# Kernel tuning notes

Measured on AMD Instinct MI355X. Metric: run time of the kernel, lower is better.

Reference implementation:

```python
import jax, jax.numpy as jnp
import numpy as np

DIM = 256
HEADS = 8
DK = DIM // HEADS
MLP_HID = 4 * DIM
EPS = 1e-5


def _ln(t, s, b):
    m = jnp.mean(t, axis=-1, keepdims=True)
    v = jnp.mean((t - m) ** 2, axis=-1, keepdims=True)
    return (t - m) / jnp.sqrt(v + EPS) * s + b


def setup_inputs() -> dict:
    key = jax.random.key(0)
    ks = jax.random.split(key, 32)
    B, N, C = 8, 128, DIM
    d = {}
    d["x"] = jax.random.normal(ks[0], (B, N, C), jnp.float32)
    d["y"] = jax.random.normal(ks[1], (B, N, N, C), jnp.float32)
    def lin(k, fi, fo):
        k1, k2 = jax.random.split(k)
        return (jax.random.normal(k1, (fi, fo), jnp.float32) * 0.02,
                jax.random.normal(k2, (fo,), jnp.float32) * 0.02)
    for i, nm in enumerate(["q", "k", "v", "e", "oe", "on"]):
        w, b = lin(ks[2 + i], C, C)
        d[f"W{nm}"], d[f"b{nm}"] = w, b
    for i, nm in enumerate(["mlp1", "mlp2"]):
        w1, b1 = lin(ks[10 + 2 * i], C, MLP_HID)
        w2, b2 = lin(ks[11 + 2 * i], MLP_HID, C)
        d[f"{nm}_w1"], d[f"{nm}_b1"] = w1, b1
        d[f"{nm}_w2"], d[f"{nm}_b2"] = w2, b2
    for i, nm in enumerate(["ln1", "ln3", "ln4", "ln5", "ln6"]):
        d[f"{nm}_s"] = jnp.ones((C,), jnp.float32)
        d[f"{nm}_b"] = jnp.zeros((C,), jnp.float32)
    return d


def reference(x, y, Wq, bq, Wk, bk, Wv, bv, We, be, Woe, boe, Won, bon,
              mlp1_w1, mlp1_b1, mlp1_w2, mlp1_b2,
              mlp2_w1, mlp2_b1, mlp2_w2, mlp2_b2,
              ln1_s, ln1_b, ln3_s, ln3_b, ln4_s, ln4_b,
              ln5_s, ln5_b, ln6_s, ln6_b):
    B, N, C = x.shape
    H, DKl = HEADS, DK

    x1 = _ln(x, ln1_s, ln1_b)

    # attention (elementwise q*k modulated by edge embeddings)
    q = (x1 @ Wq + bq).reshape(B, N, H, DKl)
    k = (x1 @ Wk + bk).reshape(B, N, H, DKl)
    v = (x1 @ Wv + bv).reshape(B, N, H, DKl)
    e = (y @ We + be).reshape(B, N, N, H, DKl)

    attn = q[:, :, None] * k[:, None, :]          # (B,N,N,H,DK)
    attn = attn / jnp.sqrt(jnp.float32(DKl))
    attn = attn * (e + 1.0) * e

    edge_out = attn.reshape(B, N, N, C) @ Woe + boe  # out_e
    p = jax.nn.softmax(attn, axis=2)                 # softmax over second n
    agg = jnp.einsum("bijhd,bjhd->bihd", p, v).reshape(B, N, C)
    node_out = agg @ Won + bon                       # out_n

    x2 = _ln(x1 + node_out, ln3_s, ln3_b)
    y2 = _ln(edge_out + y, ln4_s, ln4_b)

    mlp_x = jax.nn.relu(x2 @ mlp1_w1 + mlp1_b1) @ mlp1_w2 + mlp1_b2
    mlp_y = jax.nn.relu(y2 @ mlp2_w1 + mlp2_b1) @ mlp2_w2 + mlp2_b2

    x_out = _ln(x2 + mlp_x, ln5_s, ln5_b)
    y_out = _ln(y2 + mlp_y, ln6_s, ln6_b)
    return (x_out, y_out)
```

## Files before the change

### kernel.cpp

```cpp
#include <hip/hip_runtime.h>

#define CDIM 256
#define NSEQ 128
#define HID 1024
#define EPS 1e-5f
#define SCALE 0.17677669529663687f
#define ASTR 264
#define MROWS 32

typedef __attribute__((ext_vector_type(8))) short short8;
typedef __attribute__((ext_vector_type(4))) float f32x4;

static __device__ __forceinline__ unsigned short f2bf(float x) {
    unsigned u = __float_as_uint(x);
    u += 0x7fff + ((u >> 16) & 1);
    return (unsigned short)(u >> 16);
}
static __device__ __forceinline__ float bf2f(unsigned short h) {
    return __uint_as_float(((unsigned)h) << 16);
}

__global__ __launch_bounds__(256) void prep_all(
    const float* __restrict__ We, const float* __restrict__ Woe,
    const float* __restrict__ W1, const float* __restrict__ W2,
    unsigned short* __restrict__ WeH, unsigned short* __restrict__ WeL,
    unsigned short* __restrict__ WoH, unsigned short* __restrict__ W1H,
    unsigned short* __restrict__ W2H) {
    int blk = blockIdx.x;
    const float* W; unsigned short* H; unsigned short* L = nullptr;
    int N, ksBits, base;
    if (blk < 256)       { W = We;  H = WeH; L = WeL; N = 256;  ksBits = 3; base = 0; }
    else if (blk < 512)  { W = Woe; H = WoH; N = 256;  ksBits = 3; base = 256; }
    else if (blk < 1536) { W = W1;  H = W1H; N = 1024; ksBits = 3; base = 512; }
    else                 { W = W2;  H = W2H; N = 256;  ksBits = 5; base = 1536; }
    int idx = (blk - base) * 256 + threadIdx.x;
    int j = idx & 7, lane = (idx >> 3) & 63, rest = idx >> 9;
    int ks = rest & ((1 << ksBits) - 1), nt = rest >> ksBits;
    int n  = nt * 16 + (lane & 15);
    int kk = ks * 32 + ((lane >> 4) << 3) + j;
    float x = W[kk * N + n];
    unsigned short h = f2bf(x);
    H[idx] = h;
    if (L) L[idx] = f2bf(x - bf2f(h));
}

__global__ __launch_bounds__(256) void lnqkv_kernel(
    const float* __restrict__ x,
    const float* __restrict__ ln1s, const float* __restrict__ ln1b,
    const float* __restrict__ Wq, const float* __restrict__ bq,
    const float* __restrict__ Wk, const float* __restrict__ bk,
    const float* __restrict__ Wv, const float* __restrict__ bv,
    float* __restrict__ x1,
    float* __restrict__ q, float* __restrict__ k, float* __restrict__ v) {
    __shared__ float sX[4][CDIM];
    __shared__ float sMu[4], sRs[4];
    const int bi0 = blockIdx.x * 4, t = threadIdx.x;
    const int w = t >> 6, lane = t & 63;
    float xv[4];
    #pragma unroll
    for (int r = 0; r < 4; ++r) { xv[r] = x[(bi0 + r) * CDIM + t]; sX[r][t] = xv[r]; }
    __syncthreads();
    {
        float s = 0.f, ss = 0.f;
        #pragma unroll
        for (int m = 0; m < 4; ++m) { float a = sX[w][lane + 64 * m]; s += a; ss += a * a; }
        #pragma unroll
        for (int off = 32; off; off >>= 1) { s += __shfl_xor(s, off); ss += __shfl_xor(ss, off); }
        if (lane == 0) {
            float mu = s * (1.f / 256.f);
            sMu[w] = mu;
            sRs[w] = rsqrtf(ss * (1.f / 256.f) - mu * mu + EPS);
        }
    }
    __syncthreads();
    #pragma unroll
    for (int r = 0; r < 4; ++r) {
        float xn = (xv[r] - sMu[r]) * sRs[r] * ln1s[t] + ln1b[t];
        sX[r][t] = xn;
        x1[(bi0 + r) * CDIM + t] = xn;
    }
    __syncthreads();
    float aq[4], ak[4], av[4];
    #pragma unroll
    for (int r = 0; r < 4; ++r) { aq[r] = bq[t]; ak[r] = bk[t]; av[r] = bv[t]; }
    #pragma unroll 4
    for (int kk = 0; kk < CDIM; ++kk) {
        float wq = Wq[kk * CDIM + t], wk = Wk[kk * CDIM + t], wv = Wv[kk * CDIM + t];
        #pragma unroll
        for (int r = 0; r < 4; ++r) {
            float xd = sX[r][kk];
            aq[r] += xd * wq; ak[r] += xd * wk; av[r] += xd * wv;
        }
    }
    #pragma unroll
    for (int r = 0; r < 4; ++r) {
        q[(bi0 + r) * CDIM + t] = aq[r];
        k[(bi0 + r) * CDIM + t] = ak[r];
        v[(bi0 + r) * CDIM + t] = av[r];
    }
}

template <int TERMS>
static __device__ __forceinline__ void gemmN(
    const unsigned short* Ah, const unsigned short* Al,
    const unsigned short* __restrict__ Bh, const unsigned short* __restrict__ Bl,
    int nt0, int ksTotal, int ks0, int lane, f32x4 acc[2][2])
{
    const int l16 = lane & 15, quad = lane >> 4;
    #pragma unroll 2
    for (int ks = 0; ks < 8; ++ks) {
        short8 bh[2], bl[2];
        #pragma unroll
        for (int nt = 0; nt < 2; ++nt) {
            size_t off = ((size_t)((nt0 + nt) * ksTotal + (ks0 + ks)) * 64 + lane) * 8;
            bh[nt] = *(const short8*)(Bh + off);
            if (TERMS == 3) bl[nt] = *(const short8*)(Bl + off);
        }
        #pragma unroll
        for (int mt = 0; mt < 2; ++mt) {
            int ao = (mt * 16 + l16) * ASTR + ks * 32 + quad * 8;
            short8 ah = *(const short8*)(Ah + ao);
            short8 al = *(const short8*)(Al + ao);
            #pragma unroll
            for (int nt = 0; nt < 2; ++nt) {
                acc[mt][nt] = __builtin_amdgcn_mfma_f32_16x16x32_bf16(ah, bh[nt], acc[mt][nt], 0, 0, 0);
                acc[mt][nt] = __builtin_amdgcn_mfma_f32_16x16x32_bf16(al, bh[nt], acc[mt][nt], 0, 0, 0);
                if (TERMS == 3)
                    acc[mt][nt] = __builtin_amdgcn_mfma_f32_16x16x32_bf16(ah, bl[nt], acc[mt][nt], 0, 0, 0);
            }
        }
    }
}

static __device__ __forceinline__ void ln_reduce32(
    float pre[2][2][4], float* sSum, float* sSS, int w, int l16, int quad, int tid)
{
    #pragma unroll
    for (int mt = 0; mt < 2; ++mt)
        #pragma unroll
        for (int r = 0; r < 4; ++r) {
            float s  = pre[mt][0][r] + pre[mt][1][r];
            float ss = pre[mt][0][r] * pre[mt][0][r] + pre[mt][1][r] * pre[mt][1][r];
            #pragma unroll
            for (int off = 1; off < 16; off <<= 1) {
                s  += __shfl_xor(s, off);
                ss += __shfl_xor(ss, off);
            }
            if (l16 == 0) {
                int row = mt * 16 + quad * 4 + r;
                sSum[w * 32 + row] = s;
                sSS [w * 32 + row] = ss;
            }
        }
    __syncthreads();
    if (tid < 32) {
        float S = 0.f, SS2 = 0.f;
        #pragma unroll
        for (int ww = 0; ww < 8; ++ww) { S += sSum[ww * 32 + tid]; SS2 += sSS[ww * 32 + tid]; }
        float mu = S * (1.f / 256.f);
        float rs = rsqrtf(SS2 * (1.f / 256.f) - mu * mu + EPS);
        sSum[tid] = mu; sSS[tid] = rs;
    }
    __syncthreads();
}

__global__ __launch_bounds__(512, 4) void y_mega(
    const float* __restrict__ y, const float* __restrict__ qg, const float* __restrict__ kg,
    const unsigned short* __restrict__ WeH, const unsigned short* __restrict__ WeL,
    const float* __restrict__ be,
    const unsigned short* __restrict__ WoH, const float* __restrict__ boe,
    const unsigned short* __restrict__ W1H, const float* __restrict__ b1,
    const unsigned short* __restrict__ W2H, const float* __restrict__ b2,
    const float* __restrict__ ln4s, const float* __restrict__ ln4b,
    const float* __restrict__ ln6s, const float* __restrict__ ln6b,
    unsigned short* __restrict__ attn_bf, float* __restrict__ yout)
{
    __shared__ unsigned short sAh[MROWS * ASTR], sAl[MROWS * ASTR];
    __shared__ unsigned short sHh[MROWS * ASTR], sHl[MROWS * ASTR];
    __shared__ float sSum[8 * 32], sSS[8 * 32];

    const int tid  = threadIdx.x;
    const int w    = tid >> 6, lane = tid & 63;
    const int l16  = lane & 15, quad = lane >> 4;
    const long long row0 = (long long)blockIdx.x * MROWS;
    const int b  = (int)(row0 >> 14);
    const int i  = (int)((row0 >> 7) & 127);
    const int j0 = (int)(row0 & 127);
    const float* qrow  = qg + ((b << 7) + i) * CDIM;
    const float* kbase = kg + ((b << 7) + j0) * CDIM;
    const int c0 = w * 32 + l16, c1 = c0 + 16;

    {
        int r  = tid >> 4;
        int cc = (tid & 15) * 16;
        const float* src = y + (row0 + r) * CDIM + cc;
        unsigned short hbuf[16], lbuf[16];
        #pragma unroll
        for (int e = 0; e < 16; e += 4) {
            float4 vv = *(const float4*)(src + e);
            float a[4] = {vv.x, vv.y, vv.z, vv.w};
            #pragma unroll
            for (int d = 0; d < 4; ++d) {
                unsigned short h = f2bf(a[d]);
                hbuf[e + d] = h;
                lbuf[e + d] = f2bf(a[d] - bf2f(h));
            }
        }
        #pragma unroll
        for (int e = 0; e < 16; e += 8) {
            *(short8*)&sAh[r * ASTR + cc + e] = *(short8*)&hbuf[e];
            *(short8*)&sAl[r * ASTR + cc + e] = *(short8*)&lbuf[e];
        }
    }
    __syncthreads();

    f32x4 acc[2][2];
    const f32x4 zf = {0.f, 0.f, 0.f, 0.f};

    #pragma unroll
    for (int mt = 0; mt < 2; ++mt) { acc[mt][0] = zf; acc[mt][1] = zf; }
    gemmN<3>(sAh, sAl, WeH, WeL, w * 2, 8, 0, lane, acc);

    float q0 = qrow[c0], q1 = qrow[c1];
    float be0 = be[c0], be1 = be[c1];
    float attnv[2][2][4];
    #pragma unroll
    for (int mt = 0; mt < 2; ++mt)
        #pragma unroll
        for (int r = 0; r < 4; ++r) {
            int mloc = mt * 16 + quad * 4 + r;
            float k0 = kbase[mloc * CDIM + c0], k1 = kbase[mloc * CDIM + c1];
            float e0 = acc[mt][0][r] + be0, e1 = acc[mt][1][r] + be1;
            float a0 = q0 * k0 * SCALE * ((e0 + 1.f) * e0);
            float a1 = q1 * k1 * SCALE * ((e1 + 1.f) * e1);
            attnv[mt][0][r] = a0; attnv[mt][1][r] = a1;
            attn_bf[(row0 + mloc) * CDIM + c0] = f2bf(a0);
            attn_bf[(row0 + mloc) * CDIM + c1] = f2bf(a1);
        }
    __syncthreads();

    #pragma unroll
    for (int mt = 0; mt < 2; ++mt)
        #pragma unroll
        for (int r = 0; r < 4; ++r) {
            int mloc = mt * 16 + quad * 4 + r;
            #pragma unroll
            for (int nt = 0; nt < 2; ++nt) {
                int c = (nt == 0) ? c0 : c1;
                float a = attnv[mt][nt][r];
                unsigned short h = f2bf(a);
                sAh[mloc * ASTR + c] = h;
                sAl[mloc * ASTR + c] = f2bf(a - bf2f(h));
            }
        }
    __syncthreads();

    #pragma unroll
    for (int mt = 0; mt < 2; ++mt) { acc[mt][0] = zf; acc[mt][1] = zf; }
    gemmN<2>(sAh, sAl, WoH, nullptr, w * 2, 8, 0, lane, acc);

    float pre[2][2][4];
    float bo0 = boe[c0], bo1 = boe[c1];
    #pragma unroll
    for (int mt = 0; mt < 2; ++mt)
        #pragma unroll
        for (int r = 0; r < 4; ++r) {
            int mloc = mt * 16 + quad * 4 + r;
            pre[mt][0][r] = acc[mt][0][r] + bo0 + y[(row0 + mloc) * CDIM + c0];
            pre[mt][1][r] = acc[mt][1][r] + bo1 + y[(row0 + mloc) * CDIM + c1];
        }
    ln_reduce32(pre, sSum, sSS, w, l16, quad, tid);

    float l4s0 = ln4s[c0], l4b0 = ln4b[c0], l4s1 = ln4s[c1], l4b1 = ln4b[c1];
    float y2v[2][2][4];
    #pragma unroll
    for (int mt = 0; mt < 2; ++mt)
        #pragma unroll
        for (int r = 0; r < 4; ++r) {
            int mloc = mt * 16 + quad * 4 + r;
            float mu = sSum[mloc], rs = sSS[mloc];
            float v0 = (pre[mt][0][r] - mu) * rs * l4s0 + l4b0;
            float v1 = (pre[mt][1][r] - mu) * rs * l4s1 + l4b1;
            y2v[mt][0][r] = v0; y2v[mt][1][r] = v1;
            unsigned short h0 = f2bf(v0), h1 = f2bf(v1);
            sAh[mloc * ASTR + c0] = h0; sAl[mloc * ASTR + c0] = f2bf(v0 - bf2f(h0));
            sAh[mloc * ASTR + c1] = h1; sAl[mloc * ASTR + c1] = f2bf(v1 - bf2f(h1));
        }
    __syncthreads();

    f32x4 out[2][2];
    #pragma unroll
    for (int mt = 0; mt < 2; ++mt) { out[mt][0] = zf; out[mt][1] = zf; }
    for (int qq = 0; qq < 4; ++qq) {
        f32x4 hh[2][2];
        #pragma unroll
        for (int mt = 0; mt < 2; ++mt) { hh[mt][0] = zf; hh[mt][1] = zf; }
        gemmN<2>(sAh, sAl, W1H, nullptr, qq * 16 + w * 2, 8, 0, lane, hh);
        float bb0 = b1[qq * 256 + c0], bb1 = b1[qq * 256 + c1];
        __syncthreads();
        #pragma unroll
        for (int mt = 0; mt < 2; ++mt)
            #pragma unroll
            for (int r = 0; r < 4; ++r) {
                int mloc = mt * 16 + quad * 4 + r;
                float h0 = fmaxf(hh[mt][0][r] + bb0, 0.f);
                float h1 = fmaxf(hh[mt][1][r] + bb1, 0.f);
                unsigned short hb0 = f2bf(h0), hb1 = f2bf(h1);
                sHh[mloc * ASTR + c0] = hb0; sHl[mloc * ASTR + c0] = f2bf(h0 - bf2f(hb0));
                sHh[mloc * ASTR + c1] = hb1; sHl[mloc * ASTR + c1] = f2bf(h1 - bf2f(hb1));
            }
        __syncthreads();
        gemmN<2>(sHh, sHl, W2H, nullptr, w * 2, 32, qq * 8, lane, out);
    }

    float b20 = b2[c0], b21 = b2[c1];
    #pragma unroll
    for (int mt = 0; mt < 2; ++mt)
        #pragma unroll
        for (int r = 0; r < 4; ++r) {
            pre[mt][0][r] = y2v[mt][0][r] + out[mt][0][r] + b20;
            pre[mt][1][r] = y2v[mt][1][r] + out[mt][1][r] + b21;
        }
    ln_reduce32(pre, sSum, sSS, w, l16, quad, tid);

    float l6s0 = ln6s[c0], l6b0 = ln6b[c0], l6s1 = ln6s[c1], l6b1 = ln6b[c1];
    #pragma unroll
    for (int mt = 0; mt < 2; ++mt)
        #pragma unroll
        for (int r = 0; r < 4; ++r) {
            int mloc = mt * 16 + quad * 4 + r;
            float mu = sSum[mloc], rs = sSS[mloc];
            yout[(row0 + mloc) * CDIM + c0] = (pre[mt][0][r] - mu) * rs * l6s0 + l6b0;
            yout[(row0 + mloc) * CDIM + c1] = (pre[mt][1][r] - mu) * rs * l6s1 + l6b1;
        }
}

__global__ __launch_bounds__(256) void softmax_agg(
    const unsigned short* __restrict__ attn, const float* __restrict__ v,
    float* __restrict__ agg) {
    __shared__ float2 sM[2][128], sS[2][128], sO[2][128];
    const int bi = blockIdx.x, t = threadIdx.x;
    const int c2 = t & 127, team = t >> 7, ch = c2 * 2;
    const unsigned short* ap = attn + (size_t)bi * NSEQ * CDIM + ch;
    const float* vp = v + (size_t)(bi >> 7) * NSEQ * CDIM + ch;
    const int jb = team * 64;
    float m0 = -1e30f, m1 = -1e30f;
    #pragma unroll 4
    for (int j = jb; j < jb + 64; ++j) {
        unsigned uu = *(const unsigned*)(ap + (size_t)j * CDIM);
        m0 = fmaxf(m0, bf2f((unsigned short)uu));
        m1 = fmaxf(m1, bf2f((unsigned short)(uu >> 16)));
    }
    sM[team][c2] = make_float2(m0, m1);
    __syncthreads();
    float2 mo = sM[team ^ 1][c2];
    m0 = fmaxf(m0, mo.x); m1 = fmaxf(m1, mo.y);
    float s0 = 0.f, s1 = 0.f, o0 = 0.f, o1 = 0.f;
    #pragma unroll 4
    for (int j = jb; j < jb + 64; ++j) {
        unsigned uu = *(const unsigned*)(ap + (size_t)j * CDIM);
        float e0 = __expf(bf2f((unsigned short)uu) - m0);
        float e1 = __expf(bf2f((unsigned short)(uu >> 16)) - m1);
        float2 vv = *(const float2*)(vp + (size_t)j * CDIM);
        s0 += e0; s1 += e1;
        o0 += e0 * vv.x; o1 += e1 * vv.y;
    }
    sS[team][c2] = make_float2(s0, s1);
    sO[team][c2] = make_float2(o0, o1);
    __syncthreads();
    if (team == 0) {
        float2 s2 = sS[1][c2], o2 = sO[1][c2];
        float r0 = (o0 + o2.x) / (s0 + s2.x);
        float r1 = (o1 + o2.y) / (s1 + s2.y);
        *(float2*)(agg + (size_t)bi * CDIM + ch) = make_float2(r0, r1);
    }
}

__global__ __launch_bounds__(256) void x_path(
    const float* __restrict__ x1, const float* __restrict__ agg,
    const float* __restrict__ Won, const float* __restrict__ bon,
    const float* __restrict__ ln3s, const float* __restrict__ ln3b,
    const float* __restrict__ w1, const float* __restrict__ b1,
    const float* __restrict__ w2, const float* __restrict__ b2,
    const float* __restrict__ ln5s, const float* __restrict__ ln5b,
    float* __restrict__ xout) {
    __shared__ float sG[4][CDIM];
    __shared__ float sP[4][CDIM];
    __shared__ float sH[4][HID];
    __shared__ float sMu[4], sRs[4];
    const int bi0 = blockIdx.x * 4, t = threadIdx.x;
    const int w = t >> 6, lane = t & 63;
    #pragma unroll
    for (int r = 0; r < 4; ++r) sG[r][t] = agg[(bi0 + r) * CDIM + t];
    __syncthreads();
    float no[4];
    #pragma unroll
    for (int r = 0; r < 4; ++r) no[r] = bon[t];
    #pragma unroll 4
    for (int kk = 0; kk < CDIM; ++kk) {
        float wv = Won[kk * CDIM + t];
        #pragma unroll
        for (int r = 0; r < 4; ++r) no[r] += sG[r][kk] * wv;
    }
    float pre[4];
    #pragma unroll
    for (int r = 0; r < 4; ++r) {
        pre[r] = x1[(bi0 + r) * CDIM + t] + no[r];
        sP[r][t] = pre[r];
    }
    __syncthreads();
    {
        float s = 0.f, ss = 0.f;
        #pragma unroll
        for (int m = 0; m < 4; ++m) { float a = sP[w][lane + 64 * m]; s += a; ss += a * a; }
        #pragma unroll
        for (int off = 32; off; off >>= 1) { s += __shfl_xor(s, off); ss += __shfl_xor(ss, off); }
        if (lane == 0) {
            float mu = s * (1.f / 256.f);
            sMu[w] = mu; sRs[w] = rsqrtf(ss * (1.f / 256.f) - mu * mu + EPS);
        }
    }
    __syncthreads();
    float x2[4];
    #pragma unroll
    for (int r = 0; r < 4; ++r) {
        x2[r] = (pre[r] - sMu[r]) * sRs[r] * ln3s[t] + ln3b[t];
        sP[r][t] = x2[r];
    }
    __syncthreads();
    float h[4][4];
    #pragma unroll
    for (int m = 0; m < 4; ++m) {
        float bb = b1[t + 256 * m];
        #pragma unroll
        for (int r = 0; r < 4; ++r) h[r][m] = bb;
    }
    #pragma unroll 2
    for (int kk = 0; kk < CDIM; ++kk) {
        float wv[4];
        #pragma unroll
        for (int m = 0; m < 4; ++m) wv[m] = w1[kk * HID + t + 256 * m];
        #pragma unroll
        for (int r = 0; r < 4; ++r) {
            float xd = sP[r][kk];
            #pragma unroll
            for (int m = 0; m < 4; ++m) h[r][m] += xd * wv[m];
        }
    }
    #pragma unroll
    for (int r = 0; r < 4; ++r)
        #pragma unroll
        for (int m = 0; m < 4; ++m) sH[r][t + 256 * m] = fmaxf(h[r][m], 0.f);
    __syncthreads();
    float o[4];
    #pragma unroll
    for (int r = 0; r < 4; ++r) o[r] = b2[t];
    #pragma unroll 4
    for (int u = 0; u < HID; ++u) {
        float wv = w2[u * CDIM + t];
        #pragma unroll
        for (int r = 0; r < 4; ++r) o[r] += sH[r][u] * wv;
    }
    float pre2[4];
    #pragma unroll
    for (int r = 0; r < 4; ++r) { pre2[r] = x2[r] + o[r]; sP[r][t] = pre2[r]; }
    __syncthreads();
    {
        float s = 0.f, ss = 0.f;
        #pragma unroll
        for (int m = 0; m < 4; ++m) { float a = sP[w][lane + 64 * m]; s += a; ss += a * a; }
        #pragma unroll
        for (int off = 32; off; off >>= 1) { s += __shfl_xor(s, off); ss += __shfl_xor(ss, off); }
        if (lane == 0) {
            float mu = s * (1.f / 256.f);
            sMu[w] = mu; sRs[w] = rsqrtf(ss * (1.f / 256.f) - mu * mu + EPS);
        }
    }
    __syncthreads();
    #pragma unroll
    for (int r = 0; r < 4; ++r)
        xout[(bi0 + r) * CDIM + t] = (pre2[r] - sMu[r]) * sRs[r] * ln5s[t] + ln5b[t];
}

extern "C" void kernel_launch(void* const* d_in, const int* in_sizes, int n_in,
                              void* d_out, int out_size, void* d_ws, size_t ws_size,
                              hipStream_t stream) {
    const float* x   = (const float*)d_in[0];
    const float* y   = (const float*)d_in[1];
    const float* Wq  = (const float*)d_in[2];  const float* bq  = (const float*)d_in[3];
    const float* Wk  = (const float*)d_in[4];  const float* bk  = (const float*)d_in[5];
    const float* Wv  = (const float*)d_in[6];  const float* bv  = (const float*)d_in[7];
    const float* We  = (const float*)d_in[8];  const float* be  = (const float*)d_in[9];
    const float* Woe = (const float*)d_in[10]; const float* boe = (const float*)d_in[11];
    const float* Won = (const float*)d_in[12]; const float* bon = (const float*)d_in[13];
    const float* m1w1= (const float*)d_in[14]; const float* m1b1= (const float*)d_in[15];
    const float* m1w2= (const float*)d_in[16]; const float* m1b2= (const float*)d_in[17];
    const float* m2w1= (const float*)d_in[18]; const float* m2b1= (const float*)d_in[19];
    const float* m2w2= (const float*)d_in[20]; const float* m2b2= (const float*)d_in[21];
    const float* ln1s= (const float*)d_in[22]; const float* ln1b= (const float*)d_in[23];
    const float* ln3s= (const float*)d_in[24]; const float* ln3b= (const float*)d_in[25];
    const float* ln4s= (const float*)d_in[26]; const float* ln4b= (const float*)d_in[27];
    const float* ln5s= (const float*)d_in[28]; const float* ln5b= (const float*)d_in[29];
    const float* ln6s= (const float*)d_in[30]; const float* ln6b= (const float*)d_in[31];

    const int BN  = 8 * 128;
    const long long BNN = 8LL * 128 * 128;

    float* ws  = (float*)d_ws;
    float* x1  = ws;
    float* q   = x1 + BN * CDIM;
    float* k   = q  + BN * CDIM;
    float* v   = k  + BN * CDIM;
    float* agg = v  + BN * CDIM;
    unsigned short* attn_bf = (unsigned short*)(agg + BN * CDIM);
    unsigned short* WeH = attn_bf + BNN * CDIM;
    unsigned short* WeL = WeH + 65536;
    unsigned short* WoH = WeL + 65536;
    unsigned short* W1H = WoH + 65536;
    unsigned short* W2H = W1H + 262144;

    float* xout = (float*)d_out;
    float* yout = xout + BN * CDIM;

    prep_all<<<2560, 256, 0, stream>>>(We, Woe, m2w1, m2w2, WeH, WeL, WoH, W1H, W2H);
    lnqkv_kernel<<<BN / 4, 256, 0, stream>>>(x, ln1s, ln1b, Wq, bq, Wk, bk, Wv, bv,
                                             x1, q, k, v);
    y_mega<<<(int)(BNN / MROWS), 512, 0, stream>>>(
        y, q, k, WeH, WeL, be, WoH, boe, W1H, m2b1, W2H, m2b2,
        ln4s, ln4b, ln6s, ln6b, attn_bf, yout);
    softmax_agg<<<BN, 256, 0, stream>>>(attn_bf, v, agg);
    x_path<<<BN / 4, 256, 0, stream>>>(x1, agg, Won, bon, ln3s, ln3b,
                                       m1w1, m1b1, m1w2, m1b2, ln5s, ln5b, xout);
}
```

Measured before the change: 880.3 us.

## Compute softmax partial maxima in y_mega and split x_path reductions across 512 threads

y_mega now reduces each 32-row tile's attention values to per-channel maxima and writes them to a small workspace buffer. softmax_agg reads these four partial maxima instead of making a separate pass over the bf16 attention tensor, which removes one full read of that tensor and a barrier. x_path doubles its thread count and splits the K dimension of the Won and W2 matvecs across two halves, combining them through shared memory to raise parallelism. The max is taken from fp32 values rather than the bf16-rounded ones, so it can differ slightly from the true max of the stored data, which is harmless for softmax stability.

```diff
diff --git a/kernel.cpp b/kernel.cpp
--- a/kernel.cpp
+++ b/kernel.cpp
@@ -173,7 +173,8 @@
     const unsigned short* __restrict__ W2H, const float* __restrict__ b2,
     const float* __restrict__ ln4s, const float* __restrict__ ln4b,
     const float* __restrict__ ln6s, const float* __restrict__ ln6b,
-    unsigned short* __restrict__ attn_bf, float* __restrict__ yout)
+    unsigned short* __restrict__ attn_bf, float* __restrict__ pmax,
+    float* __restrict__ yout)
 {
     __shared__ unsigned short sAh[MROWS * ASTR], sAl[MROWS * ASTR];
     __shared__ unsigned short sHh[MROWS * ASTR], sHl[MROWS * ASTR];
@@ -237,6 +238,26 @@
             attn_bf[(row0 + mloc) * CDIM + c0] = f2bf(a0);
             attn_bf[(row0 + mloc) * CDIM + c1] = f2bf(a1);
         }
+
+    {
+        float mx0 = -1e30f, mx1 = -1e30f;
+        #pragma unroll
+        for (int mt = 0; mt < 2; ++mt)
+            #pragma unroll
+            for (int r = 0; r < 4; ++r) {
+                mx0 = fmaxf(mx0, attnv[mt][0][r]);
+                mx1 = fmaxf(mx1, attnv[mt][1][r]);
+            }
+        mx0 = fmaxf(mx0, __shfl_xor(mx0, 16));
+        mx0 = fmaxf(mx0, __shfl_xor(mx0, 32));
+        mx1 = fmaxf(mx1, __shfl_xor(mx1, 16));
+        mx1 = fmaxf(mx1, __shfl_xor(mx1, 32));
+        if (quad == 0) {
+            float* pm = pmax + ((size_t)((b << 7) + i) * 4 + (j0 >> 5)) * CDIM;
+            pm[c0] = mx0;
+            pm[c1] = mx1;
+        }
+    }
     __syncthreads();
 
     #pragma unroll
@@ -337,26 +358,22 @@
 
 __global__ __launch_bounds__(256) void softmax_agg(
     const unsigned short* __restrict__ attn, const float* __restrict__ v,
-    float* __restrict__ agg) {
-    __shared__ float2 sM[2][128], sS[2][128], sO[2][128];
+    const float* __restrict__ pmax, float* __restrict__ agg) {
+    __shared__ float2 sS[2][128], sO[2][128];
     const int bi = blockIdx.x, t = threadIdx.x;
     const int c2 = t & 127, team = t >> 7, ch = c2 * 2;
     const unsigned short* ap = attn + (size_t)bi * NSEQ * CDIM + ch;
     const float* vp = v + (size_t)(bi >> 7) * NSEQ * CDIM + ch;
+    const float* mp = pmax + (size_t)bi * 4 * CDIM + ch;
+    float2 mv0 = *(const float2*)(mp);
+    float2 mv1 = *(const float2*)(mp + CDIM);
+    float2 mv2 = *(const float2*)(mp + 2 * CDIM);
+    float2 mv3 = *(const float2*)(mp + 3 * CDIM);
+    float m0 = fmaxf(fmaxf(mv0.x, mv1.x), fmaxf(mv2.x, mv3.x));
+    float m1 = fmaxf(fmaxf(mv0.y, mv1.y), fmaxf(mv2.y, mv3.y));
     const int jb = team * 64;
-    float m0 = -1e30f, m1 = -1e30f;
-    #pragma unroll 4
-    for (int j = jb; j < jb + 64; ++j) {
-        unsigned uu = *(const unsigned*)(ap + (size_t)j * CDIM);
-        m0 = fmaxf(m0, bf2f((unsigned short)uu));
-        m1 = fmaxf(m1, bf2f((unsigned short)(uu >> 16)));
-    }
-    sM[team][c2] = make_float2(m0, m1);
-    __syncthreads();
-    float2 mo = sM[team ^ 1][c2];
-    m0 = fmaxf(m0, mo.x); m1 = fmaxf(m1, mo.y);
     float s0 = 0.f, s1 = 0.f, o0 = 0.f, o1 = 0.f;
-    #pragma unroll 4
+    #pragma unroll 8
     for (int j = jb; j < jb + 64; ++j) {
         unsigned uu = *(const unsigned*)(ap + (size_t)j * CDIM);
         float e0 = __expf(bf2f((unsigned short)uu) - m0);
@@ -376,7 +393,7 @@
     }
 }
 
-__global__ __launch_bounds__(256) void x_path(
+__global__ __launch_bounds__(512) void x_path(
     const float* __restrict__ x1, const float* __restrict__ agg,
     const float* __restrict__ Won, const float* __restrict__ bon,
     const float* __restrict__ ln3s, const float* __restrict__ ln3b,
@@ -387,29 +404,36 @@
     __shared__ float sG[4][CDIM];
     __shared__ float sP[4][CDIM];
     __shared__ float sH[4][HID];
+    __shared__ float sR[2][4][CDIM];
     __shared__ float sMu[4], sRs[4];
     const int bi0 = blockIdx.x * 4, t = threadIdx.x;
+    const int ct = t & 255, hs = t >> 8;
     const int w = t >> 6, lane = t & 63;
     #pragma unroll
-    for (int r = 0; r < 4; ++r) sG[r][t] = agg[(bi0 + r) * CDIM + t];
-    __syncthreads();
-    float no[4];
-    #pragma unroll
-    for (int r = 0; r < 4; ++r) no[r] = bon[t];
+    for (int p = 0; p < 2; ++p) {
+        int idx = p * 512 + t;
+        ((float*)sG)[idx] = agg[bi0 * CDIM + idx];
+    }
+    __syncthreads();
+    float no[4] = {0.f, 0.f, 0.f, 0.f};
+    const int k0 = hs * 128;
     #pragma unroll 4
-    for (int kk = 0; kk < CDIM; ++kk) {
-        float wv = Won[kk * CDIM + t];
+    for (int kk = k0; kk < k0 + 128; ++kk) {
+        float wv = Won[kk * CDIM + ct];
         #pragma unroll
         for (int r = 0; r < 4; ++r) no[r] += sG[r][kk] * wv;
     }
+    #pragma unroll
+    for (int r = 0; r < 4; ++r) sR[hs][r][ct] = no[r];
+    __syncthreads();
     float pre[4];
     #pragma unroll
     for (int r = 0; r < 4; ++r) {
-        pre[r] = x1[(bi0 + r) * CDIM + t] + no[r];
-        sP[r][t] = pre[r];
-    }
-    __syncthreads();
-    {
+        pre[r] = x1[(bi0 + r) * CDIM + ct] + bon[ct] + sR[0][r][ct] + sR[1][r][ct];
+        if (hs == 0) sP[r][ct] = pre[r];
+    }
+    __syncthreads();
+    if (w < 4) {
         float s = 0.f, ss = 0.f;
         #pragma unroll
         for (int m = 0; m < 4; ++m) { float a = sP[w][lane + 64 * m]; s += a; ss += a * a; }
@@ -424,48 +448,50 @@
     float x2[4];
     #pragma unroll
     for (int r = 0; r < 4; ++r) {
-        x2[r] = (pre[r] - sMu[r]) * sRs[r] * ln3s[t] + ln3b[t];
-        sP[r][t] = x2[r];
-    }
-    __syncthreads();
-    float h[4][4];
-    #pragma unroll
-    for (int m = 0; m < 4; ++m) {
-        float bb = b1[t + 256 * m];
-        #pragma unroll
-        for (int r = 0; r < 4; ++r) h[r][m] = bb;
+        x2[r] = (pre[r] - sMu[r]) * sRs[r] * ln3s[ct] + ln3b[ct];
+        if (hs == 0) sP[r][ct] = x2[r];
+    }
+    __syncthreads();
+    float h0[4], h1[4];
+    {
+        float bb0 = b1[t], bb1 = b1[t + 512];
+        #pragma unroll
+        for (int r = 0; r < 4; ++r) { h0[r] = bb0; h1[r] = bb1; }
     }
     #pragma unroll 2
     for (int kk = 0; kk < CDIM; ++kk) {
-        float wv[4];
-        #pragma unroll
-        for (int m = 0; m < 4; ++m) wv[m] = w1[kk * HID + t + 256 * m];
+        float wv0 = w1[kk * HID + t], wv1 = w1[kk * HID + t + 512];
         #pragma unroll
         for (int r = 0; r < 4; ++r) {
             float xd = sP[r][kk];
-            #pragma unroll
-            for (int m = 0; m < 4; ++m) h[r][m] += xd * wv[m];
-        }
-    }
-    #pragma unroll
-    for (int r = 0; r < 4; ++r)
-        #pragma unroll
-        for (int m = 0; m < 4; ++m) sH[r][t + 256 * m] = fmaxf(h[r][m], 0.f);
-    __syncthreads();
-    float o[4];
-    #pragma unroll
-    for (int r = 0; r < 4; ++r) o[r] = b2[t];
+            h0[r] += xd * wv0; h1[r] += xd * wv1;
+        }
+    }
+    #pragma unroll
+    for (int r = 0; r < 4; ++r) {
+        sH[r][t]       = fmaxf(h0[r], 0.f);
+        sH[r][t + 512] = fmaxf(h1[r], 0.f);
+    }
+    __syncthreads();
+    float o[4] = {0.f, 0.f, 0.f, 0.f};
+    const int u0 = hs * 512;
     #pragma unroll 4
-    for (int u = 0; u < HID; ++u) {
-        float wv = w2[u * CDIM + t];
+    for (int u = u0; u < u0 + 512; ++u) {
+        float wv = w2[u * CDIM + ct];
         #pragma unroll
         for (int r = 0; r < 4; ++r) o[r] += sH[r][u] * wv;
     }
+    #pragma unroll
+    for (int r = 0; r < 4; ++r) sR[hs][r][ct] = o[r];
+    __syncthreads();
     float pre2[4];
     #pragma unroll
-    for (int r = 0; r < 4; ++r) { pre2[r] = x2[r] + o[r]; sP[r][t] = pre2[r]; }
-    __syncthreads();
-    {
+    for (int r = 0; r < 4; ++r) {
+        pre2[r] = x2[r] + b2[ct] + sR[0][r][ct] + sR[1][r][ct];
+        if (hs == 0) sP[r][ct] = pre2[r];
+    }
+    __syncthreads();
+    if (w < 4) {
         float s = 0.f, ss = 0.f;
         #pragma unroll
         for (int m = 0; m < 4; ++m) { float a = sP[w][lane + 64 * m]; s += a; ss += a * a; }
@@ -477,9 +503,10 @@
         }
     }
     __syncthreads();
-    #pragma unroll
-    for (int r = 0; r < 4; ++r)
-        xout[(bi0 + r) * CDIM + t] = (pre2[r] - sMu[r]) * sRs[r] * ln5s[t] + ln5b[t];
+    if (hs == 0)
+        #pragma unroll
+        for (int r = 0; r < 4; ++r)
+            xout[(bi0 + r) * CDIM + ct] = (pre2[r] - sMu[r]) * sRs[r] * ln5s[ct] + ln5b[ct];
 }
 
 extern "C" void kernel_launch(void* const* d_in, const int* in_sizes, int n_in,
@@ -518,6 +545,7 @@
     unsigned short* WoH = WeL + 65536;
     unsigned short* W1H = WoH + 65536;
     unsigned short* W2H = W1H + 262144;
+    float* pmax = (float*)(W2H + 262144);
 
     float* xout = (float*)d_out;
     float* yout = xout + BN * CDIM;
@@ -527,8 +555,8 @@
                                              x1, q, k, v);
     y_mega<<<(int)(BNN / MROWS), 512, 0, stream>>>(
         y, q, k, WeH, WeL, be, WoH, boe, W1H, m2b1, W2H, m2b2,
-        ln4s, ln4b, ln6s, ln6b, attn_bf, yout);
-    softmax_agg<<<BN, 256, 0, stream>>>(attn_bf, v, agg);
-    x_path<<<BN / 4, 256, 0, stream>>>(x1, agg, Won, bon, ln3s, ln3b,
+        ln4s, ln4b, ln6s, ln6b, attn_bf, pmax, yout);
+    softmax_agg<<<BN, 256, 0, stream>>>(attn_bf, v, pmax, agg);
+    x_path<<<BN / 4, 512, 0, stream>>>(x1, agg, Won, bon, ln3s, ln3b,
                                        m1w1, m1b1, m1w2, m1b2, ln5s, ln5b, xout);
 }
```

Measured after the change: 805.4 us. 1.09x faster.
